# Performance work log

Measured on AMD Instinct MI355X. Metric: run time of the kernel, lower is better.

Reference implementation:

```python
import jax, jax.numpy as jnp
import numpy as np

N_NODES = 100_000
N_CH = 16
DIM = 3
N_EDGES = 1_600_000
N_STEPS = 2
MAX_STEP_LEN = 1.0
EPS = jnp.float32(jnp.finfo(jnp.float32).eps)  # orig uses float64 eps; fp32-safe here


def setup_inputs() -> dict:
    key = jax.random.key(0)
    k1, k2, k3, k4, k5 = jax.random.split(key, 5)
    nodes = jax.random.normal(k1, (N_NODES, N_CH, DIM), dtype=jnp.float32)
    nodes = nodes / jnp.linalg.norm(nodes, axis=-1, keepdims=True)  # project to S^2
    senders = jax.random.randint(k2, (N_EDGES,), 0, N_NODES, dtype=jnp.int32)
    receivers = jax.random.randint(k3, (N_EDGES,), 0, N_NODES, dtype=jnp.int32)
    weights = jnp.ones((N_EDGES,), dtype=jnp.float32)
    # mimic truncated_normal(std=1)+1 inits (squared later => positive params)
    t_sqrt = 1.0 + 0.5 * jax.random.normal(k4, (N_CH,), dtype=jnp.float32)
    alpha_sqrt = 1.0 + 0.5 * jax.random.normal(k5, (N_CH,), dtype=jnp.float32)
    beta_sqrt = jnp.ones((N_CH,), dtype=jnp.float32)
    return dict(nodes=nodes, senders=senders, receivers=receivers, weights=weights,
                t_sqrt=t_sqrt, alpha_sqrt=alpha_sqrt, beta_sqrt=beta_sqrt)


def sphere_log(x, y):
    # log_x(y) on the unit sphere; x, y: (..., DIM)
    c = jnp.clip(jnp.sum(x * y, axis=-1, keepdims=True), -1.0 + 1e-7, 1.0 - 1e-7)
    theta = jnp.arccos(c)
    return (theta / jnp.sin(theta)) * (y - c * x)


def sphere_exp(x, v):
    # exp_x(v) on the unit sphere
    n = jnp.sqrt(jnp.sum(v * v, axis=-1, keepdims=True) + 1e-16)
    return jnp.cos(n) * x + (jnp.sin(n) / n) * v


def mfdg_laplace(nodes, senders, receivers, weights):
    # degree-normalized manifold graph Laplacian:
    #   L(x)_i = -(1/deg_i) * sum_{j in N(i)} w_ij log_{x_i}(x_j)
    logs = sphere_log(nodes[senders], nodes[receivers])         # (E, C, D)
    agg = jax.ops.segment_sum(weights[:, None, None] * logs, senders,
                              num_segments=N_NODES)             # (N, C, D)
    deg = jax.ops.segment_sum(weights, senders, num_segments=N_NODES)
    return -agg / (deg[:, None, None] + 1e-12)


def _flow(nodes, senders, receivers, weights, t_sqrt, alpha_sqrt, beta_sqrt):
    t = (t_sqrt ** 2) / N_STEPS   # (C,)
    a = alpha_sqrt ** 2           # (C,)
    b = beta_sqrt ** 2            # (C,)
    x = nodes
    for _ in range(N_STEPS):
        v = mfdg_laplace(x, senders, receivers, weights)        # (N, C, D)
        nrm = jnp.sqrt(jnp.sum(v * v, axis=-1) + EPS)           # (N, C)
        d = jax.nn.sigmoid(b * (nrm - a))                       # sigmoid gating
        scale = jnp.where(nrm * d <= MAX_STEP_LEN, d, MAX_STEP_LEN / nrm)
        v = -(v * scale[..., None]) * t[None, :, None]
        x = sphere_exp(x, v)
    return x


def reference(nodes, senders, receivers, weights, t_sqrt, alpha_sqrt, beta_sqrt):
    return _flow(nodes, senders, receivers, weights, t_sqrt, alpha_sqrt, beta_sqrt)
```

## Files before the change

kernel.cpp:

```cpp
#include <hip/hip_runtime.h>

#define N_NODES 100000
#define N_CH 16
#define DIM 3
#define N_EDGES 1600000
#define N_STEPS 2
#define EPS_D 1.1920928955078125e-7

#define PB 1024
#define NBLK ((N_NODES + PB - 1) / PB)
#define DBINS 64

__global__ void hist_kernel(const int4* __restrict__ senders4,
                            int* __restrict__ cnt) {
    int e = blockIdx.x * blockDim.x + threadIdx.x;
    if (e < N_EDGES / 4) {
        int4 s = senders4[e];
        atomicAdd(&cnt[s.x], 1);
        atomicAdd(&cnt[s.y], 1);
        atomicAdd(&cnt[s.z], 1);
        atomicAdd(&cnt[s.w], 1);
    }
}

__global__ void scan_partials_dhist(const int* __restrict__ cnt,
                                    int* __restrict__ part,
                                    int* __restrict__ bins) {
    __shared__ int sh[PB];
    __shared__ int lb[DBINS];
    int t = threadIdx.x;
    if (t < DBINS) lb[t] = 0;
    int g = blockIdx.x * PB + t;
    int v = (g < N_NODES) ? cnt[g] : 0;
    sh[t] = v;
    __syncthreads();
    for (int off = PB / 2; off > 0; off >>= 1) {
        if (t < off) sh[t] += sh[t + off];
        __syncthreads();
    }
    if (t == 0) part[blockIdx.x] = sh[0];
    if (g < N_NODES) {
        int d = (v > DBINS - 1) ? (DBINS - 1) : v;
        atomicAdd(&lb[d], 1);
    }
    __syncthreads();
    if (t < DBINS && lb[t]) atomicAdd(&bins[t], lb[t]);
}

__global__ void scan_mid_fused(int* __restrict__ part,
                               int* __restrict__ rowptr,
                               const int* __restrict__ bins,
                               int* __restrict__ binoff,
                               int* __restrict__ binfill) {
    __shared__ int sh[128];
    int t = threadIdx.x;
    int v = (t < NBLK) ? part[t] : 0;
    sh[t] = v;
    __syncthreads();
    for (int off = 1; off < 128; off <<= 1) {
        int u = (t >= off) ? sh[t - off] : 0;
        __syncthreads();
        sh[t] += u;
        __syncthreads();
    }
    if (t < NBLK) part[t] = sh[t] - v;
    if (t == NBLK - 1) rowptr[N_NODES] = sh[t];
    if (t < DBINS) {
        int bv = bins[t];
        int s = bv;
        for (int off = 1; off < DBINS; off <<= 1) {
            int u = __shfl_up(s, off, 64);
            if (t >= off) s += u;
        }
        binoff[t] = s - bv;
        binfill[t] = 0;
    }
}

__global__ void scan_apply_dscatter(const int* __restrict__ cnt,
                                    const int* __restrict__ part,
                                    int* __restrict__ rowptr,
                                    const int* __restrict__ binoff,
                                    int* __restrict__ binfill,
                                    int* __restrict__ perm) {
    __shared__ int sh[PB];
    __shared__ int lcnt[DBINS];
    __shared__ int lbase[DBINS];
    int t = threadIdx.x;
    if (t < DBINS) lcnt[t] = 0;
    int g = blockIdx.x * PB + t;
    int v = (g < N_NODES) ? cnt[g] : 0;
    sh[t] = v;
    __syncthreads();
    for (int off = 1; off < PB; off <<= 1) {
        int u = (t >= off) ? sh[t - off] : 0;
        __syncthreads();
        sh[t] += u;
        __syncthreads();
    }
    if (g < N_NODES) rowptr[g] = part[blockIdx.x] + sh[t] - v;
    int d = 0, myoff = 0;
    if (g < N_NODES) {
        d = (v > DBINS - 1) ? (DBINS - 1) : v;
        myoff = atomicAdd(&lcnt[d], 1);
    }
    __syncthreads();
    if (t < DBINS && lcnt[t]) lbase[t] = atomicAdd(&binfill[t], lcnt[t]);
    __syncthreads();
    if (g < N_NODES && perm) perm[binoff[d] + lbase[d] + myoff] = g;
}

__global__ void scatter_kernel(const int* __restrict__ senders,
                               const int* __restrict__ receivers,
                               const float* __restrict__ weights,
                               const int* __restrict__ rowptr,
                               int* __restrict__ cnt,
                               int2* __restrict__ edata) {
    int e = blockIdx.x * blockDim.x + threadIdx.x;
    if (e >= N_EDGES) return;
    int s = senders[e];
    int old = atomicAdd(&cnt[s], -1);
    edata[rowptr[s] + old - 1] = make_int2(receivers[e], __float_as_int(weights[e]));
}

__device__ __forceinline__ double fast_rsqrt(double x) {
    double y = (double)rsqrtf((float)x);
    y = y * fma(-0.5 * x, y * y, 1.5);
    return y;
}

__device__ __forceinline__ double theta_over_sin(double cd) {
    double acd = fabs(cd);
    bool mid = (acd <= 0.5);
    double z = mid ? (cd * cd) : (0.5 * (1.0 - acd));
    double A = 0.008390335809943149;
    A = fma(A, z, 0.009761609529194078);
    A = fma(A, z, 0.011551800896139706);
    A = fma(A, z, 0.013964843750);
    A = fma(A, z, 0.017352764423076924);
    A = fma(A, z, 0.022372159090909092);
    A = fma(A, z, 0.030381944444444444);
    A = fma(A, z, 0.044642857142857144);
    A = fma(A, z, 0.075);
    A = fma(A, z, 0.16666666666666666);
    A = fma(A, z, 1.0);
    double R = fast_rsqrt(1.0 - z);
    if (mid) return (1.5707963267948966 - cd * A) * R;
    double AR = A * R;
    if (cd > 0.0) return AR;
    double Rz = fast_rsqrt(z);
    return fma(1.5707963267948966 * Rz, R, -AR);
}

template <typename TI, typename TO>
__global__ void flow_kernel(const TI* __restrict__ x,
                            const int* __restrict__ rowptr,
                            const int2* __restrict__ edata,
                            const int* __restrict__ perm,
                            const float* __restrict__ t_sqrt,
                            const float* __restrict__ alpha_sqrt,
                            const float* __restrict__ beta_sqrt,
                            TO* __restrict__ xout) {
    int wave = threadIdx.x >> 6;
    int lane = threadIdx.x & 63;
    int q = lane >> 4;
    int c = lane & 15;
    int slot = (blockIdx.x * 4 + wave) * 4 + q;
    int i = perm ? perm[slot] : slot;

    int beg = rowptr[i];
    int end = rowptr[i + 1];

    const TI* xi = x + ((size_t)i * N_CH + c) * DIM;
    double ax = (double)xi[0], ay = (double)xi[1], az = (double)xi[2];

    double sx = 0.0, sy = 0.0, sz = 0.0, sw = 0.0;
    for (int k = beg; k < end; ++k) {
        int2 ed = edata[k];
        int r = ed.x;
        double w = (double)__int_as_float(ed.y);
        const TI* xr = x + ((size_t)r * N_CH + c) * DIM;
        double bx = (double)xr[0], by = (double)xr[1], bz = (double)xr[2];

        double cd = ax * bx + ay * by + az * bz;
        cd = fmin(fmax(cd, -1.0 + 1e-7), 1.0 - 1e-7);
        double f = w * theta_over_sin(cd);

        sx += f * (bx - cd * ax);
        sy += f * (by - cd * ay);
        sz += f * (bz - cd * az);
        sw += w;
    }

    double dg = sw + 1e-12;
    double inv = 1.0 / dg;
    double vx = -sx * inv, vy = -sy * inv, vz = -sz * inv;

    double t = (double)t_sqrt[c];     t = (t * t) / (double)N_STEPS;
    double a = (double)alpha_sqrt[c]; a = a * a;
    double b = (double)beta_sqrt[c];  b = b * b;

    double nrm = sqrt(vx * vx + vy * vy + vz * vz + EPS_D);
    double d = 1.0 / (1.0 + exp(-b * (nrm - a)));
    double scale = (nrm * d <= 1.0) ? d : (1.0 / nrm);
    double fs = -scale * t;
    vx *= fs; vy *= fs; vz *= fs;

    double n = sqrt(vx * vx + vy * vy + vz * vz + 1e-16);
    double cn = cos(n);
    double sf = sin(n) / n;

    TO* xo = xout + ((size_t)i * N_CH + c) * DIM;
    xo[0] = (TO)(cn * ax + sf * vx);
    xo[1] = (TO)(cn * ay + sf * vy);
    xo[2] = (TO)(cn * az + sf * vz);
}

__global__ void deg_kernel(const int* __restrict__ senders,
                           const float* __restrict__ weights,
                           float* __restrict__ deg) {
    int e = blockIdx.x * blockDim.x + threadIdx.x;
    if (e < N_EDGES) atomicAdd(&deg[senders[e]], weights[e]);
}

__global__ void edge_kernel(const float* __restrict__ x,
                            const int* __restrict__ senders,
                            const int* __restrict__ receivers,
                            const float* __restrict__ weights,
                            float* __restrict__ agg) {
    unsigned int tid = blockIdx.x * blockDim.x + threadIdx.x;
    if (tid >= (unsigned int)N_EDGES * N_CH) return;
    unsigned int e = tid >> 4;
    unsigned int c = tid & 15u;
    int s = senders[e];
    int r = receivers[e];
    float w = weights[e];
    const float* xs = x + ((size_t)s * N_CH + c) * DIM;
    const float* xr = x + ((size_t)r * N_CH + c) * DIM;
    float ax = xs[0], ay = xs[1], az = xs[2];
    float bx = xr[0], by = xr[1], bz = xr[2];
    float cd = ax * bx + ay * by + az * bz;
    cd = fminf(fmaxf(cd, -1.0f + 1e-7f), 1.0f - 1e-7f);
    float theta = acosf(cd);
    float sn = sqrtf(fmaxf(1.0f - cd * cd, 0.0f));
    float f = w * theta / sn;
    float* ag = agg + ((size_t)s * N_CH + c) * DIM;
    atomicAdd(&ag[0], f * (bx - cd * ax));
    atomicAdd(&ag[1], f * (by - cd * ay));
    atomicAdd(&ag[2], f * (bz - cd * az));
}

__global__ void node_kernel(const float* __restrict__ xin,
                            const float* __restrict__ agg,
                            const float* __restrict__ deg,
                            const float* __restrict__ t_sqrt,
                            const float* __restrict__ alpha_sqrt,
                            const float* __restrict__ beta_sqrt,
                            float* __restrict__ xout) {
    unsigned int tid = blockIdx.x * blockDim.x + threadIdx.x;
    if (tid >= (unsigned int)N_NODES * N_CH) return;
    unsigned int i = tid >> 4;
    unsigned int c = tid & 15u;
    float dg = deg[i] + 1e-12f;
    const float* ag = agg + (size_t)tid * DIM;
    float vx = -ag[0] / dg, vy = -ag[1] / dg, vz = -ag[2] / dg;
    float t = t_sqrt[c]; t = (t * t) * (1.0f / N_STEPS);
    float a = alpha_sqrt[c]; a = a * a;
    float b = beta_sqrt[c]; b = b * b;
    float nrm = sqrtf(vx * vx + vy * vy + vz * vz + 1.1920929e-7f);
    float d = 1.0f / (1.0f + __expf(-b * (nrm - a)));
    float scale = (nrm * d <= 1.0f) ? d : (1.0f / nrm);
    float fs = -scale * t;
    vx *= fs; vy *= fs; vz *= fs;
    const float* xi = xin + (size_t)tid * DIM;
    float axx = xi[0], ayy = xi[1], azz = xi[2];
    float n = sqrtf(vx * vx + vy * vy + vz * vz + 1e-16f);
    float cn = cosf(n);
    float sf = sinf(n) / n;
    float* xo = xout + (size_t)tid * DIM;
    xo[0] = cn * axx + sf * vx;
    xo[1] = cn * ayy + sf * vy;
    xo[2] = cn * azz + sf * vz;
}

extern "C" void kernel_launch(void* const* d_in, const int* in_sizes, int n_in,
                              void* d_out, int out_size, void* d_ws, size_t ws_size,
                              hipStream_t stream) {
    const float* nodes      = (const float*)d_in[0];
    const int*   senders    = (const int*)d_in[1];
    const int*   receivers  = (const int*)d_in[2];
    const float* weights    = (const float*)d_in[3];
    const float* t_sqrt     = (const float*)d_in[4];
    const float* alpha_sqrt = (const float*)d_in[5];
    const float* beta_sqrt  = (const float*)d_in[6];
    float* out = (float*)d_out;

    const size_t AL = 255;
    const size_t xtmp_b   = (size_t)N_NODES * N_CH * DIM * sizeof(double);
    const size_t rowptr_b = (((size_t)(N_NODES + 1) * sizeof(int)) + AL) & ~AL;
    const size_t cnt_b    = (((size_t)N_NODES * sizeof(int)) + AL) & ~AL;
    const size_t bins_b   = 1024;
    const size_t part_b   = 4096;
    const size_t perm_b   = (((size_t)N_NODES * sizeof(int)) + AL) & ~AL;
    const size_t edata_b  = (size_t)N_EDGES * sizeof(int2);
    const size_t need_sorted = xtmp_b + rowptr_b + cnt_b + bins_b + part_b + perm_b + edata_b;
    const size_t need_plain  = xtmp_b + rowptr_b + cnt_b + bins_b + part_b + edata_b;

    if (ws_size >= need_plain) {
        bool sorted = (ws_size >= need_sorted);
        char* p = (char*)d_ws;
        double* xtmp  = (double*)p;           p += xtmp_b;
        int*   rowptr = (int*)p;              p += rowptr_b;
        int*   cnt    = (int*)p;              p += cnt_b;
        int*   bins   = (int*)p;
        int*   binoff = bins + 64;
        int*   binfill= bins + 128;           p += bins_b;
        int*   part   = (int*)p;              p += part_b;
        int*   perm   = nullptr;
        if (sorted) { perm = (int*)p;         p += perm_b; }
        int2*  edata  = (int2*)p;

        hipMemsetAsync(cnt, 0, cnt_b + 256, stream);
        hist_kernel<<<(N_EDGES / 4 + 255) / 256, 256, 0, stream>>>(
            (const int4*)senders, cnt);
        scan_partials_dhist<<<NBLK, PB, 0, stream>>>(cnt, part, bins);
        scan_mid_fused<<<1, 128, 0, stream>>>(part, rowptr, bins, binoff, binfill);
        scan_apply_dscatter<<<NBLK, PB, 0, stream>>>(cnt, part, rowptr,
                                                     binoff, binfill, perm);
        scatter_kernel<<<(N_EDGES + 255) / 256, 256, 0, stream>>>(
            senders, receivers, weights, rowptr, cnt, edata);

        int grid = N_NODES / 16;
        flow_kernel<float, double><<<grid, 256, 0, stream>>>(
            nodes, rowptr, edata, perm, t_sqrt, alpha_sqrt, beta_sqrt, xtmp);
        flow_kernel<double, float><<<grid, 256, 0, stream>>>(
            xtmp, rowptr, edata, perm, t_sqrt, alpha_sqrt, beta_sqrt, out);
    } else {
        float* agg = (float*)d_ws;
        float* deg = agg + (size_t)N_NODES * N_CH * DIM;
        hipMemsetAsync(deg, 0, N_NODES * sizeof(float), stream);
        deg_kernel<<<(N_EDGES + 255) / 256, 256, 0, stream>>>(senders, weights, deg);
        const float* xin = nodes;
        for (int step = 0; step < N_STEPS; ++step) {
            hipMemsetAsync(agg, 0, (size_t)N_NODES * N_CH * DIM * sizeof(float), stream);
            unsigned int n_ec = (unsigned int)N_EDGES * N_CH;
            edge_kernel<<<(n_ec + 255) / 256, 256, 0, stream>>>(xin, senders, receivers,
                                                                weights, agg);
            unsigned int n_nc = (unsigned int)N_NODES * N_CH;
            node_kernel<<<(n_nc + 255) / 256, 256, 0, stream>>>(xin, agg, deg, t_sqrt,
                                                                alpha_sqrt, beta_sqrt, out);
            xin = out;
        }
    }
}
```

Measured before the change: 381.6 us.

## Replace random CSR edge scatter with two-pass coarse bucket then fine scatter

Edges are first partitioned into 256 coarse buckets of 512 senders each, written to a staging buffer that reuses the xtmp workspace. A second pass then scatters within each bucket's local region into the CSR edge array. The aim is to make the atomics and writes of the final scatter land in a small, cache-resident address range instead of spreading randomly over the whole array. The cost is an extra full pass over edge data plus staging traffic. It also relies on bfill being initialised from rowptr at 512-node boundaries, and on 196 buckets fitting within 256.

```diff
diff --git a/kernel.cpp b/kernel.cpp
--- a/kernel.cpp
+++ b/kernel.cpp
@@ -10,6 +10,10 @@
 #define PB 1024
 #define NBLK ((N_NODES + PB - 1) / PB)
 #define DBINS 64
+#define NBUCK 256
+#define TA 4096
+#define NBLK_A ((N_EDGES + TA - 1) / TA)
+#define NBLK_B 2048
 
 __global__ void hist_kernel(const int4* __restrict__ senders4,
                             int* __restrict__ cnt) {
@@ -82,7 +86,8 @@
                                     int* __restrict__ rowptr,
                                     const int* __restrict__ binoff,
                                     int* __restrict__ binfill,
-                                    int* __restrict__ perm) {
+                                    int* __restrict__ perm,
+                                    int* __restrict__ bfill) {
     __shared__ int sh[PB];
     __shared__ int lcnt[DBINS];
     __shared__ int lbase[DBINS];
@@ -98,7 +103,11 @@
         sh[t] += u;
         __syncthreads();
     }
-    if (g < N_NODES) rowptr[g] = part[blockIdx.x] + sh[t] - v;
+    if (g < N_NODES) {
+        int rp = part[blockIdx.x] + sh[t] - v;
+        rowptr[g] = rp;
+        if ((g & 511) == 0) bfill[g >> 9] = rp;
+    }
     int d = 0, myoff = 0;
     if (g < N_NODES) {
         d = (v > DBINS - 1) ? (DBINS - 1) : v;
@@ -110,17 +119,55 @@
     if (g < N_NODES && perm) perm[binoff[d] + lbase[d] + myoff] = g;
 }
 
-__global__ void scatter_kernel(const int* __restrict__ senders,
+__global__ void bucket_scatter(const int* __restrict__ senders,
                                const int* __restrict__ receivers,
                                const float* __restrict__ weights,
-                               const int* __restrict__ rowptr,
-                               int* __restrict__ cnt,
-                               int2* __restrict__ edata) {
-    int e = blockIdx.x * blockDim.x + threadIdx.x;
-    if (e >= N_EDGES) return;
-    int s = senders[e];
-    int old = atomicAdd(&cnt[s], -1);
-    edata[rowptr[s] + old - 1] = make_int2(receivers[e], __float_as_int(weights[e]));
+                               int* __restrict__ bfill,
+                               int* __restrict__ stg_s,
+                               int2* __restrict__ stg_rw) {
+    __shared__ int lcnt[NBUCK];
+    __shared__ int lbase[NBUCK];
+    int t = threadIdx.x;
+    lcnt[t] = 0;
+    __syncthreads();
+    int base = blockIdx.x * TA;
+    for (int k = t; k < TA; k += 256) {
+        int e = base + k;
+        if (e < N_EDGES) atomicAdd(&lcnt[senders[e] >> 9], 1);
+    }
+    __syncthreads();
+    int c = lcnt[t];
+    if (c) lbase[t] = atomicAdd(&bfill[t], c);
+    __syncthreads();
+    lcnt[t] = 0;
+    __syncthreads();
+    for (int k = t; k < TA; k += 256) {
+        int e = base + k;
+        if (e < N_EDGES) {
+            int s = senders[e];
+            int b = s >> 9;
+            int pos = lbase[b] + atomicAdd(&lcnt[b], 1);
+            stg_s[pos] = s;
+            stg_rw[pos] = make_int2(receivers[e], __float_as_int(weights[e]));
+        }
+    }
+}
+
+__global__ void fine_scatter(const int* __restrict__ stg_s,
+                             const int2* __restrict__ stg_rw,
+                             const int* __restrict__ rowptr,
+                             int* __restrict__ cnt,
+                             int2* __restrict__ edata) {
+    const int CH = (N_EDGES + NBLK_B - 1) / NBLK_B;
+    int bid = blockIdx.x;
+    int chunk = (bid & 7) * (NBLK_B / 8) + (bid >> 3);
+    int s0 = chunk * CH;
+    int s1 = s0 + CH; if (s1 > N_EDGES) s1 = N_EDGES;
+    for (int e = s0 + (int)threadIdx.x; e < s1; e += 256) {
+        int s = stg_s[e];
+        int old = atomicAdd(&cnt[s], -1);
+        edata[rowptr[s] + old - 1] = stg_rw[e];
+    }
 }
 
 __device__ __forceinline__ double fast_rsqrt(double x) {
@@ -299,7 +346,7 @@
     const size_t xtmp_b   = (size_t)N_NODES * N_CH * DIM * sizeof(double);
     const size_t rowptr_b = (((size_t)(N_NODES + 1) * sizeof(int)) + AL) & ~AL;
     const size_t cnt_b    = (((size_t)N_NODES * sizeof(int)) + AL) & ~AL;
-    const size_t bins_b   = 1024;
+    const size_t bins_b   = 2048;
     const size_t part_b   = 4096;
     const size_t perm_b   = (((size_t)N_NODES * sizeof(int)) + AL) & ~AL;
     const size_t edata_b  = (size_t)N_EDGES * sizeof(int2);
@@ -314,11 +361,15 @@
         int*   cnt    = (int*)p;              p += cnt_b;
         int*   bins   = (int*)p;
         int*   binoff = bins + 64;
-        int*   binfill= bins + 128;           p += bins_b;
+        int*   binfill= bins + 128;
+        int*   bfill  = bins + 192;           p += bins_b;
         int*   part   = (int*)p;              p += part_b;
         int*   perm   = nullptr;
         if (sorted) { perm = (int*)p;         p += perm_b; }
         int2*  edata  = (int2*)p;
+
+        int2*  stg_rw = (int2*)xtmp;
+        int*   stg_s  = (int*)((char*)xtmp + edata_b);
 
         hipMemsetAsync(cnt, 0, cnt_b + 256, stream);
         hist_kernel<<<(N_EDGES / 4 + 255) / 256, 256, 0, stream>>>(
@@ -326,9 +377,10 @@
         scan_partials_dhist<<<NBLK, PB, 0, stream>>>(cnt, part, bins);
         scan_mid_fused<<<1, 128, 0, stream>>>(part, rowptr, bins, binoff, binfill);
         scan_apply_dscatter<<<NBLK, PB, 0, stream>>>(cnt, part, rowptr,
-                                                     binoff, binfill, perm);
-        scatter_kernel<<<(N_EDGES + 255) / 256, 256, 0, stream>>>(
-            senders, receivers, weights, rowptr, cnt, edata);
+                                                     binoff, binfill, perm, bfill);
+        bucket_scatter<<<NBLK_A, NBUCK, 0, stream>>>(senders, receivers, weights,
+                                                     bfill, stg_s, stg_rw);
+        fine_scatter<<<NBLK_B, 256, 0, stream>>>(stg_s, stg_rw, rowptr, cnt, edata);
 
         int grid = N_NODES / 16;
         flow_kernel<float, double><<<grid, 256, 0, stream>>>(
```

New measurement: 354.7 us. 1.08x faster.
